# Kernel tuning notes

Hardware: AMD Instinct MI355X
Metric: run time of the kernel (lower is better)

Reference implementation:

```python
import jax, jax.numpy as jnp
import numpy as np

B, I, H = 16384, 512, 512


def _linear_params(key, out_dim, in_dim):
    kw, kb = jax.random.split(key)
    bound = 1.0 / np.sqrt(in_dim)
    W = jax.random.uniform(kw, (out_dim, in_dim), jnp.float32, -bound, bound)
    b = jax.random.uniform(kb, (out_dim,), jnp.float32, -bound, bound)
    return W, b


def setup_inputs() -> dict:
    key = jax.random.key(0)
    ks = jax.random.split(key, 12)
    x = jax.random.normal(ks[0], (B, I), jnp.float32)
    h_prev = jax.random.normal(ks[1], (B, H), jnp.float32)
    c_prev = jax.random.normal(ks[2], (B, H), jnp.float32)
    W_xi, b_xi = _linear_params(ks[3], H, I)
    W_hi, b_hi = _linear_params(ks[4], H, H)
    W_xf, b_xf = _linear_params(ks[5], H, I)
    W_hf, b_hf = _linear_params(ks[6], H, H)
    W_xc, b_xc = _linear_params(ks[7], H, I)
    W_hc, b_hc = _linear_params(ks[8], H, H)
    W_xo, b_xo = _linear_params(ks[9], H, I)
    W_ho, b_ho = _linear_params(ks[10], H, H)
    W_e, b_e = _linear_params(ks[11], H, I + H)
    return dict(x=x, h_prev=h_prev, c_prev=c_prev,
                W_xi=W_xi, b_xi=b_xi, W_hi=W_hi, b_hi=b_hi,
                W_xf=W_xf, b_xf=b_xf, W_hf=W_hf, b_hf=b_hf,
                W_xc=W_xc, b_xc=b_xc, W_hc=W_hc, b_hc=b_hc,
                W_xo=W_xo, b_xo=b_xo, W_ho=W_ho, b_ho=b_ho,
                W_e=W_e, b_e=b_e)


def reference(x, h_prev, c_prev,
              W_xi, b_xi, W_hi, b_hi,
              W_xf, b_xf, W_hf, b_hf,
              W_xc, b_xc, W_hc, b_hc,
              W_xo, b_xo, W_ho, b_ho,
              W_e, b_e):
    # Batch the 4 input-to-hidden projections into one GEMM and the 4
    # hidden-to-hidden projections into another (same math as 8 Linears).
    Wx = jnp.concatenate([W_xi, W_xf, W_xc, W_xo], axis=0)   # [4H, I]
    bx = jnp.concatenate([b_xi, b_xf, b_xc, b_xo], axis=0)   # [4H]
    Wh = jnp.concatenate([W_hi, W_hf, W_hc, W_ho], axis=0)   # [4H, H]
    bh = jnp.concatenate([b_hi, b_hf, b_hc, b_ho], axis=0)
    gates = (x @ Wx.T + bx) + (h_prev @ Wh.T + bh)            # [B, 4H]
    gi, gf, gc, go = jnp.split(gates, 4, axis=-1)
    i = jax.nn.sigmoid(gi)
    f = jax.nn.sigmoid(gf)
    g = jnp.tanh(gc)
    o = jax.nn.sigmoid(go)
    c = f * c_prev + i * g
    # exp gate: Linear on [x, h_prev] -> tanh -> exp; split W_e to avoid concat
    We_x, We_h = W_e[:, :x.shape[-1]], W_e[:, x.shape[-1]:]
    exp_factor = jnp.exp(jnp.tanh(x @ We_x.T + h_prev @ We_h.T + b_e))
    h = o * jnp.tanh(c) * exp_factor
    return (h, c)
```

## Files before the change

### kernel.cpp

```cpp
#include <hip/hip_runtime.h>
#include <stdint.h>

#define Bsz 16384
#define Hh  512
#define Kd  1024
#define BM  128
#define BNJ 32
#define BK  32
#define NT  32

typedef __attribute__((ext_vector_type(8))) short bf16x8;
typedef __attribute__((ext_vector_type(4))) float f32x4;
typedef __attribute__((ext_vector_type(8))) unsigned short u16x8;

__device__ __forceinline__ unsigned short f2bf(float f) {
    union { float f; unsigned u; } v; v.f = f;
    unsigned u = v.u;
    return (unsigned short)((u + 0x7fffu + ((u >> 16) & 1u)) >> 16);
}
__device__ __forceinline__ float fast_tanh(float x) {
    float e = __expf(2.f * x);
    return (e - 1.f) / (e + 1.f);
}
__device__ __forceinline__ float fast_sigmoid(float x) {
    return 1.f / (1.f + __expf(-x));
}

__global__ void pack_A(const float* __restrict__ x, const float* __restrict__ h,
                       unsigned short* __restrict__ A) {
    const long total = (long)Bsz * Kd / 8;
    for (long i = (long)blockIdx.x * blockDim.x + threadIdx.x; i < total;
         i += (long)gridDim.x * blockDim.x) {
        int  l    = (int)(i & 63);
        long blk  = i >> 6;
        int  u    = (int)(blk & 7);
        int  t    = (int)((blk >> 3) & 31);
        long mblk = blk >> 8;
        long row  = mblk * 128 + u * 16 + (l & 15);
        int  k0   = t * 32 + ((l >> 4) << 3);
        const float* src = (k0 < 512) ? (x + row * 512 + k0)
                                      : (h + row * 512 + (k0 - 512));
        float4 f0 = *(const float4*)(src);
        float4 f1 = *(const float4*)(src + 4);
        u16x8 o;
        o[0]=f2bf(f0.x); o[1]=f2bf(f0.y); o[2]=f2bf(f0.z); o[3]=f2bf(f0.w);
        o[4]=f2bf(f1.x); o[5]=f2bf(f1.y); o[6]=f2bf(f1.z); o[7]=f2bf(f1.w);
        *(u16x8*)(A + (i << 3)) = o;
    }
}

__global__ void pack_B(const float* __restrict__ Wxi, const float* __restrict__ Whi,
                       const float* __restrict__ Wxf, const float* __restrict__ Whf,
                       const float* __restrict__ Wxc, const float* __restrict__ Whc,
                       const float* __restrict__ Wxo, const float* __restrict__ Who,
                       const float* __restrict__ We,
                       const float* __restrict__ bxi, const float* __restrict__ bhi,
                       const float* __restrict__ bxf, const float* __restrict__ bhf,
                       const float* __restrict__ bxc, const float* __restrict__ bhc,
                       const float* __restrict__ bxo, const float* __restrict__ bho,
                       const float* __restrict__ be,
                       unsigned short* __restrict__ Bp, float* __restrict__ bias) {
    const long id = (long)blockIdx.x * blockDim.x + threadIdx.x;
    if (id < 327680) {
        int blk = (int)(id >> 6);
        int l   = (int)(id & 63);
        int kh  = blk & 1;
        int kt  = (blk >> 1) & 15;
        int rest = blk >> 5;
        int g    = rest % 5;
        int jgrp = rest / 5;
        int j  = jgrp * 16 + (l & 15);
        int k0 = kt * 64 + kh * 32 + ((l >> 4) << 3);
        const float* src;
        if (g == 4) {
            src = We + (long)j * 1024 + k0;
        } else {
            const float* Wx = (g == 0) ? Wxi : (g == 1) ? Wxf : (g == 2) ? Wxc : Wxo;
            const float* Wh = (g == 0) ? Whi : (g == 1) ? Whf : (g == 2) ? Whc : Who;
            src = (k0 < 512) ? (Wx + (long)j * 512 + k0)
                             : (Wh + (long)j * 512 + (k0 - 512));
        }
        float4 f0 = *(const float4*)(src);
        float4 f1 = *(const float4*)(src + 4);
        u16x8 o;
        o[0]=f2bf(f0.x); o[1]=f2bf(f0.y); o[2]=f2bf(f0.z); o[3]=f2bf(f0.w);
        o[4]=f2bf(f1.x); o[5]=f2bf(f1.y); o[6]=f2bf(f1.z); o[7]=f2bf(f1.w);
        *(u16x8*)(Bp + (long)blk * 512 + l * 8) = o;
    }
    if (id < 2560) {
        int row = (int)id;
        int g = row >> 9, j = row & 511;
        float b;
        if (g == 4) b = be[j];
        else {
            const float* bx = (g == 0) ? bxi : (g == 1) ? bxf : (g == 2) ? bxc : bxo;
            const float* bh = (g == 0) ? bhi : (g == 1) ? bhf : (g == 2) ? bhc : bho;
            b = bx[j] + bh[j];
        }
        bias[row] = b;
    }
}

#define GL16(g, l) __builtin_amdgcn_global_load_lds( \
    (const __attribute__((address_space(1))) unsigned int*)(g), \
    (__attribute__((address_space(3))) unsigned int*)(l), 16, 0, 0)

#define VM_I(n)    asm volatile("s_waitcnt vmcnt(" #n ")" ::: "memory")
#define VM(n)      VM_I(n)
#define BARRIER()  asm volatile("s_barrier" ::: "memory")

#define MF(a, b, c) __builtin_amdgcn_mfma_f32_16x16x32_bf16(a, b, c, 0, 0, 0)

#define RDB5(RBO) do { \
    bq0 = *(const bf16x8*)(bRP + (RBO) + 0 * 1024); \
    bq1 = *(const bf16x8*)(bRP + (RBO) + 1 * 1024); \
    bq2 = *(const bf16x8*)(bRP + (RBO) + 2 * 1024); \
    bq3 = *(const bf16x8*)(bRP + (RBO) + 3 * 1024); \
    bq4 = *(const bf16x8*)(bRP + (RBO) + 4 * 1024); \
} while (0)

#define MF4(S, BQ, G) \
    acc[G][0] = MF(a##S##0, BQ, acc[G][0]); \
    acc[G][1] = MF(a##S##1, BQ, acc[G][1]); \
    acc[G][2] = MF(a##S##2, BQ, acc[G][2]); \
    acc[G][3] = MF(a##S##3, BQ, acc[G][3]);

#define MFMA20(S) do { \
    __builtin_amdgcn_s_setprio(1); \
    MF4(S, bq0, 0) MF4(S, bq1, 1) MF4(S, bq2, 2) MF4(S, bq3, 3) MF4(S, bq4, 4) \
    __builtin_amdgcn_s_setprio(0); \
} while (0)

#define LOADA4(S, T) do { \
    asm volatile("global_load_dwordx4 %0, %1, off" : "=v"(a##S##0) : "v"(asrc + (T) * 4096L + 0 * 512)); \
    asm volatile("global_load_dwordx4 %0, %1, off" : "=v"(a##S##1) : "v"(asrc + (T) * 4096L + 1 * 512)); \
    asm volatile("global_load_dwordx4 %0, %1, off" : "=v"(a##S##2) : "v"(asrc + (T) * 4096L + 2 * 512)); \
    asm volatile("global_load_dwordx4 %0, %1, off" : "=v"(a##S##3) : "v"(asrc + (T) * 4096L + 3 * 512)); \
} while (0)

#define SGB3(SBO, T) do { \
    GL16(bsg0 + (T) * 512, lds_raw + (SBO) + bdo0); \
    GL16(bsg1 + (T) * 512, lds_raw + (SBO) + bdo1); \
    GL16(bsg2 + (T) * 512, lds_raw + (SBO) + bdo2); \
} while (0)

#define STEP(T, S, RBO, SBO) do { \
    SGB3(SBO, (T) + 1); \
    RDB5(RBO); \
    MFMA20(S); \
    LOADA4(S, (T) + 2); \
    VM(4); BARRIER(); \
} while (0)

__global__ __launch_bounds__(256, 3)
void xlstm_gemm(const unsigned short* __restrict__ Apk,
                const unsigned short* __restrict__ Bp,
                const float* __restrict__ bias,
                const float* __restrict__ c_prev,
                float* __restrict__ out) {
    __shared__ __align__(16) unsigned char lds_raw[20480];

    const int tid  = threadIdx.x;
    const int wid  = tid >> 6;
    const int lane = tid & 63;
    const int wm   = wid >> 1;
    const int wj   = wid & 1;
    const int fr   = lane & 15;
    const int q    = lane >> 4;

    const int orig = blockIdx.x;
    const int wg   = (orig & 7) * 256 + (orig >> 3);
    const int mblk = wg >> 4;
    const int jblk = wg & 15;
    const long brow = (long)mblk * BM;
    const int  bcol = jblk * BNJ;

    f32x4 acc[5][4];
#pragma unroll
    for (int g = 0; g < 5; ++g)
#pragma unroll
        for (int m = 0; m < 4; ++m)
#pragma unroll
            for (int r = 0; r < 4; ++r) acc[g][m][r] = 0.f;

    bf16x8 aP0, aP1, aP2, aP3;
    bf16x8 aQ0, aQ1, aQ2, aQ3;
    bf16x8 bq0, bq1, bq2, bq3, bq4;

    const unsigned short* asrc = Apk + (long)mblk * 131072 + wm * 2048 + lane * 8;

    const unsigned char* bRP = lds_raw + wj * 5120 + lane * 16;

    const unsigned short *bsg0, *bsg1, *bsg2;
    int bdo0, bdo1, bdo2;
#define BSTG_INIT(i) do { \
    int u_ = wid + 4 * (i); if (u_ >= 10) u_ -= 10; \
    int jl_ = u_ / 5; int g_ = u_ - 5 * jl_; \
    bsg##i = Bp + (long)(jblk * 2 + jl_) * 81920 + g_ * 16384 + lane * 8; \
    bdo##i = u_ * 1024 + lane * 16; \
} while (0)
    BSTG_INIT(0); BSTG_INIT(1); BSTG_INIT(2);
#undef BSTG_INIT

    SGB3(0, 0);
    LOADA4(P, 0);
    LOADA4(Q, 1);
    VM(4);
    BARRIER();

    for (int t = 0; t < 30; t += 2) {
        STEP(t,     P, 0,     10240);
        STEP(t + 1, Q, 10240, 0);
    }
    SGB3(10240, 31);
    RDB5(0);
    MFMA20(P);
    VM(0); BARRIER();
    RDB5(10240);
    MFMA20(Q);

    const int j = bcol + wj * 16 + fr;
    const float bi_ = bias[j];
    const float bf_ = bias[512 + j];
    const float bc_ = bias[1024 + j];
    const float bo_ = bias[1536 + j];
    const float be_ = bias[2048 + j];
    const long mbase = brow + wm * 64 + (q << 2);
#pragma unroll
    for (int m = 0; m < 4; ++m) {
#pragma unroll
        for (int r = 0; r < 4; ++r) {
            long row = mbase + m * 16 + r;
            float gi = acc[0][m][r] + bi_;
            float gf = acc[1][m][r] + bf_;
            float gc = acc[2][m][r] + bc_;
            float go = acc[3][m][r] + bo_;
            float ge = acc[4][m][r] + be_;
            float iv = fast_sigmoid(gi);
            float fv = fast_sigmoid(gf);
            float gv = fast_tanh(gc);
            float ov = fast_sigmoid(go);
            float ef = __expf(fast_tanh(ge));
            float cp = c_prev[row * 512 + j];
            float cv = fv * cp + iv * gv;
            float hv = ov * fast_tanh(cv) * ef;
            out[row * 512 + j] = hv;
            out[(long)Bsz * 512 + row * 512 + j] = cv;
        }
    }
}

extern "C" void kernel_launch(void* const* d_in, const int* in_sizes, int n_in,
                              void* d_out, int out_size, void* d_ws, size_t ws_size,
                              hipStream_t stream) {
    const float* x      = (const float*)d_in[0];
    const float* h_prev = (const float*)d_in[1];
    const float* c_prev = (const float*)d_in[2];
    const float* Wxi = (const float*)d_in[3];
    const float* bxi = (const float*)d_in[4];
    const float* Whi = (const float*)d_in[5];
    const float* bhi = (const float*)d_in[6];
    const float* Wxf = (const float*)d_in[7];
    const float* bxf = (const float*)d_in[8];
    const float* Whf = (const float*)d_in[9];
    const float* bhf = (const float*)d_in[10];
    const float* Wxc = (const float*)d_in[11];
    const float* bxc = (const float*)d_in[12];
    const float* Whc = (const float*)d_in[13];
    const float* bhc = (const float*)d_in[14];
    const float* Wxo = (const float*)d_in[15];
    const float* bxo = (const float*)d_in[16];
    const float* Who = (const float*)d_in[17];
    const float* bho = (const float*)d_in[18];
    const float* We  = (const float*)d_in[19];
    const float* be  = (const float*)d_in[20];

    unsigned short* Abf  = (unsigned short*)d_ws;
    unsigned short* Bp   = (unsigned short*)((char*)d_ws + 33554432);
    float*          bias = (float*)((char*)d_ws + 33554432 + 5242880);

    pack_A<<<2048, 256, 0, stream>>>(x, h_prev, Abf);
    pack_B<<<1280, 256, 0, stream>>>(Wxi, Whi, Wxf, Whf, Wxc, Whc, Wxo, Who, We,
                                     bxi, bhi, bxf, bhf, bxc, bhc, bxo, bho, be,
                                     Bp, bias);
    xlstm_gemm<<<2048, 256, 0, stream>>>(Abf, Bp, bias, c_prev, (float*)d_out);
}
```

Before: 118.5 us.

## Load B fragments directly from global into registers, drop LDS staging and barriers

Removes the LDS staging of B tiles, along with the global_load_lds calls, barriers, manual waitcnt and setprio. Each wave now loads its own B fragments straight from global memory into registers, double-buffered alongside A. The block-to-tile mapping is also changed so the eight XCDs share j-blocks and spread m-blocks. The aim is to cut synchronisation and LDS traffic, at the cost of each wave pair redundantly fetching B and more global load pressure. It also hands scheduling and wait placement over to the compiler.

```diff
diff --git a/kernel.cpp b/kernel.cpp
--- a/kernel.cpp
+++ b/kernel.cpp
@@ -101,22 +101,22 @@
     }
 }
 
-#define GL16(g, l) __builtin_amdgcn_global_load_lds( \
-    (const __attribute__((address_space(1))) unsigned int*)(g), \
-    (__attribute__((address_space(3))) unsigned int*)(l), 16, 0, 0)
-
-#define VM_I(n)    asm volatile("s_waitcnt vmcnt(" #n ")" ::: "memory")
-#define VM(n)      VM_I(n)
-#define BARRIER()  asm volatile("s_barrier" ::: "memory")
 
 #define MF(a, b, c) __builtin_amdgcn_mfma_f32_16x16x32_bf16(a, b, c, 0, 0, 0)
 
-#define RDB5(RBO) do { \
-    bq0 = *(const bf16x8*)(bRP + (RBO) + 0 * 1024); \
-    bq1 = *(const bf16x8*)(bRP + (RBO) + 1 * 1024); \
-    bq2 = *(const bf16x8*)(bRP + (RBO) + 2 * 1024); \
-    bq3 = *(const bf16x8*)(bRP + (RBO) + 3 * 1024); \
-    bq4 = *(const bf16x8*)(bRP + (RBO) + 4 * 1024); \
+#define LDA4(S, T) do { \
+    a##S##0 = *(const bf16x8*)(asrc + (T) * 4096 + 0 * 512); \
+    a##S##1 = *(const bf16x8*)(asrc + (T) * 4096 + 1 * 512); \
+    a##S##2 = *(const bf16x8*)(asrc + (T) * 4096 + 2 * 512); \
+    a##S##3 = *(const bf16x8*)(asrc + (T) * 4096 + 3 * 512); \
+} while (0)
+
+#define LDB5(S, T) do { \
+    b##S##0 = *(const bf16x8*)(bsrc + (T) * 512 + 0 * 16384); \
+    b##S##1 = *(const bf16x8*)(bsrc + (T) * 512 + 1 * 16384); \
+    b##S##2 = *(const bf16x8*)(bsrc + (T) * 512 + 2 * 16384); \
+    b##S##3 = *(const bf16x8*)(bsrc + (T) * 512 + 3 * 16384); \
+    b##S##4 = *(const bf16x8*)(bsrc + (T) * 512 + 4 * 16384); \
 } while (0)
 
 #define MF4(S, BQ, G) \
@@ -126,30 +126,8 @@
     acc[G][3] = MF(a##S##3, BQ, acc[G][3]);
 
 #define MFMA20(S) do { \
-    __builtin_amdgcn_s_setprio(1); \
-    MF4(S, bq0, 0) MF4(S, bq1, 1) MF4(S, bq2, 2) MF4(S, bq3, 3) MF4(S, bq4, 4) \
-    __builtin_amdgcn_s_setprio(0); \
-} while (0)
-
-#define LOADA4(S, T) do { \
-    asm volatile("global_load_dwordx4 %0, %1, off" : "=v"(a##S##0) : "v"(asrc + (T) * 4096L + 0 * 512)); \
-    asm volatile("global_load_dwordx4 %0, %1, off" : "=v"(a##S##1) : "v"(asrc + (T) * 4096L + 1 * 512)); \
-    asm volatile("global_load_dwordx4 %0, %1, off" : "=v"(a##S##2) : "v"(asrc + (T) * 4096L + 2 * 512)); \
-    asm volatile("global_load_dwordx4 %0, %1, off" : "=v"(a##S##3) : "v"(asrc + (T) * 4096L + 3 * 512)); \
-} while (0)
-
-#define SGB3(SBO, T) do { \
-    GL16(bsg0 + (T) * 512, lds_raw + (SBO) + bdo0); \
-    GL16(bsg1 + (T) * 512, lds_raw + (SBO) + bdo1); \
-    GL16(bsg2 + (T) * 512, lds_raw + (SBO) + bdo2); \
-} while (0)
-
-#define STEP(T, S, RBO, SBO) do { \
-    SGB3(SBO, (T) + 1); \
-    RDB5(RBO); \
-    MFMA20(S); \
-    LOADA4(S, (T) + 2); \
-    VM(4); BARRIER(); \
+    MF4(S, b##S##0, 0) MF4(S, b##S##1, 1) MF4(S, b##S##2, 2) \
+    MF4(S, b##S##3, 3) MF4(S, b##S##4, 4) \
 } while (0)
 
 __global__ __launch_bounds__(256, 3)
@@ -158,8 +136,6 @@
                 const float* __restrict__ bias,
                 const float* __restrict__ c_prev,
                 float* __restrict__ out) {
-    __shared__ __align__(16) unsigned char lds_raw[20480];
-
     const int tid  = threadIdx.x;
     const int wid  = tid >> 6;
     const int lane = tid & 63;
@@ -169,9 +145,10 @@
     const int q    = lane >> 4;
 
     const int orig = blockIdx.x;
-    const int wg   = (orig & 7) * 256 + (orig >> 3);
-    const int mblk = wg >> 4;
-    const int jblk = wg & 15;
+    const int xcd  = orig & 7;
+    const int oid  = orig >> 3;
+    const int jblk = oid >> 4;
+    const int mblk = (oid & 15) * 8 + xcd;
     const long brow = (long)mblk * BM;
     const int  bcol = jblk * BNJ;
 
@@ -183,40 +160,26 @@
 #pragma unroll
             for (int r = 0; r < 4; ++r) acc[g][m][r] = 0.f;
 
-    bf16x8 aP0, aP1, aP2, aP3;
-    bf16x8 aQ0, aQ1, aQ2, aQ3;
-    bf16x8 bq0, bq1, bq2, bq3, bq4;
+    bf16x8 aP0, aP1, aP2, aP3, bP0, bP1, bP2, bP3, bP4;
+    bf16x8 aQ0, aQ1, aQ2, aQ3, bQ0, bQ1, bQ2, bQ3, bQ4;
 
     const unsigned short* asrc = Apk + (long)mblk * 131072 + wm * 2048 + lane * 8;
-
-    const unsigned char* bRP = lds_raw + wj * 5120 + lane * 16;
-
-    const unsigned short *bsg0, *bsg1, *bsg2;
-    int bdo0, bdo1, bdo2;
-#define BSTG_INIT(i) do { \
-    int u_ = wid + 4 * (i); if (u_ >= 10) u_ -= 10; \
-    int jl_ = u_ / 5; int g_ = u_ - 5 * jl_; \
-    bsg##i = Bp + (long)(jblk * 2 + jl_) * 81920 + g_ * 16384 + lane * 8; \
-    bdo##i = u_ * 1024 + lane * 16; \
-} while (0)
-    BSTG_INIT(0); BSTG_INIT(1); BSTG_INIT(2);
-#undef BSTG_INIT
-
-    SGB3(0, 0);
-    LOADA4(P, 0);
-    LOADA4(Q, 1);
-    VM(4);
-    BARRIER();
-
-    for (int t = 0; t < 30; t += 2) {
-        STEP(t,     P, 0,     10240);
-        STEP(t + 1, Q, 10240, 0);
-    }
-    SGB3(10240, 31);
-    RDB5(0);
+    const unsigned short* bsrc = Bp + (long)(jblk * 2 + wj) * 81920 + lane * 8;
+
+    LDA4(P, 0); LDB5(P, 0);
+    LDA4(Q, 1); LDB5(Q, 1);
+
+    for (int t = 0; t < 28; t += 2) {
+        MFMA20(P);
+        LDA4(P, t + 2); LDB5(P, t + 2);
+        MFMA20(Q);
+        LDA4(Q, t + 3); LDB5(Q, t + 3);
+    }
     MFMA20(P);
-    VM(0); BARRIER();
-    RDB5(10240);
+    LDA4(P, 30); LDB5(P, 30);
+    MFMA20(Q);
+    LDA4(Q, 31); LDB5(Q, 31);
+    MFMA20(P);
     MFMA20(Q);
 
     const int j = bcol + wj * 16 + fr;
```

Measured after the change: 164.2 us. +38.6%, slower.
